# Kernel optimization log

Hardware: AMD Instinct MI355X
Metric: run time of the kernel (lower is better)

The kernel has to match this reference:

```python
import jax, jax.numpy as jnp
import numpy as np

EMBED_DIM = 1024
NUM_HEADS = 16
HEAD_DIM = EMBED_DIM // NUM_HEADS


def setup_inputs() -> dict:
    key = jax.random.key(0)
    ks = jax.random.split(key, 9)
    s = 1.0 / np.sqrt(EMBED_DIM)
    x = jax.random.normal(ks[0], (2, 2048, EMBED_DIM), dtype=jnp.float32)
    Wq = jax.random.uniform(ks[1], (EMBED_DIM, EMBED_DIM), jnp.float32, -s, s)
    bq = jax.random.uniform(ks[2], (EMBED_DIM,), jnp.float32, -s, s)
    Wk = jax.random.uniform(ks[3], (EMBED_DIM, EMBED_DIM), jnp.float32, -s, s)
    bk = jax.random.uniform(ks[4], (EMBED_DIM,), jnp.float32, -s, s)
    Wv = jax.random.uniform(ks[5], (EMBED_DIM, EMBED_DIM), jnp.float32, -s, s)
    bv = jax.random.uniform(ks[6], (EMBED_DIM,), jnp.float32, -s, s)
    Wo = jax.random.uniform(ks[7], (EMBED_DIM, EMBED_DIM), jnp.float32, -s, s)
    bo = jax.random.uniform(ks[8], (EMBED_DIM,), jnp.float32, -s, s)
    return {"x": x, "Wq": Wq, "bq": bq, "Wk": Wk, "bk": bk,
            "Wv": Wv, "bv": bv, "Wo": Wo, "bo": bo}


def reference(x, Wq, bq, Wk, bk, Wv, bv, Wo, bo):
    B, S, E = x.shape
    H, D = NUM_HEADS, HEAD_DIM
    # Linear projections (torch Linear: y = x @ W.T + b; here W stored as [in,out])
    Q = (x @ Wq + bq).reshape(B, S, H, D).transpose(0, 2, 1, 3)  # [B,H,S,D]
    K = (x @ Wk + bk).reshape(B, S, H, D).transpose(0, 2, 1, 3)
    V = (x @ Wv + bv).reshape(B, S, H, D).transpose(0, 2, 1, 3)
    scale = jnp.sqrt(jnp.asarray(D, dtype=jnp.float32))
    energy = jnp.einsum("bhqd,bhkd->bhqk", Q, K) / scale  # [B,H,S,S]
    attn = jax.nn.softmax(energy, axis=-1)
    out = jnp.einsum("bhqk,bhkd->bhqd", attn, V)  # [B,H,S,D]
    out = out.transpose(0, 2, 1, 3).reshape(B, S, E)
    return out @ Wo + bo
```

## Files before the change

### kernel.cpp

```cpp
#include <hip/hip_runtime.h>
#include <cstdint>
#include <cstddef>

#define S_LEN 2048
#define NHEAD 16
#define HDIM  64
#define EMB   1024
#define MROWS 4096
#define KDIM  1024

typedef __bf16 bf16;
typedef unsigned int u32;
typedef __attribute__((ext_vector_type(8)))  __bf16 bf16x8;
typedef __attribute__((ext_vector_type(4)))  __bf16 bf16x4;
typedef __attribute__((ext_vector_type(4)))  float  f32x4;
typedef __attribute__((ext_vector_type(16))) float  f32x16;
typedef __attribute__((ext_vector_type(4)))  u32    u32x4;

__device__ __forceinline__ f32x4 mfma_16x16x32(bf16x8 a, bf16x8 b, f32x4 c) {
  return __builtin_amdgcn_mfma_f32_16x16x32_bf16(a, b, c, 0, 0, 0);
}
__device__ __forceinline__ f32x16 mfma32(bf16x8 a, bf16x8 b, f32x16 c) {
  return __builtin_amdgcn_mfma_f32_32x32x16_bf16(a, b, c, 0, 0, 0);
}
__device__ __forceinline__ u32 cvt_pk_bf16(float lo, float hi) {
  u32 r;
  asm("v_cvt_pk_bf16_f32 %0, %1, %2" : "=v"(r) : "v"(lo), "v"(hi));
  return r;
}
__device__ __forceinline__ f32x16 fz16() {
  f32x16 z;
#pragma unroll
  for (int i = 0; i < 16; i++) z[i] = 0.f;
  return z;
}

__device__ __forceinline__ void gload16(const bf16* g, void* lds_uniform) {
  __builtin_amdgcn_global_load_lds(
      (const __attribute__((address_space(1))) void*)g,
      (__attribute__((address_space(3))) void*)lds_uniform, 16, 0, 0);
}

__global__ void prep_x_kernel(const float* __restrict__ x, bf16* __restrict__ xb) {
  int idx = blockIdx.x * blockDim.x + threadIdx.x;
  const float4* x4 = (const float4*)x;
  float4 a = x4[idx * 2 + 0];
  float4 b = x4[idx * 2 + 1];
  bf16x8 v;
  v[0] = (bf16)a.x; v[1] = (bf16)a.y; v[2] = (bf16)a.z; v[3] = (bf16)a.w;
  v[4] = (bf16)b.x; v[5] = (bf16)b.y; v[6] = (bf16)b.z; v[7] = (bf16)b.w;
  *(bf16x8*)(xb + (size_t)idx * 8) = v;
}

__global__ void prep_w_kernel(const float* __restrict__ Wq, const float* __restrict__ Wk,
                              const float* __restrict__ Wv, const float* __restrict__ Wo,
                              bf16* __restrict__ wqkvt, bf16* __restrict__ wot) {
  __shared__ float tile[64][65];
  int mat = blockIdx.z;
  const float* W = (mat == 0) ? Wq : (mat == 1) ? Wk : (mat == 2) ? Wv : Wo;
  bf16* dst = (mat < 3) ? (wqkvt + (size_t)mat * 1024 * 1024) : wot;
  int k0 = blockIdx.x * 64, r0 = blockIdx.y * 64;
  int tid = threadIdx.x;
#pragma unroll
  for (int i = 0; i < 16; i++) {
    int idx = i * 256 + tid;
    int kk = idx >> 6, rr = idx & 63;
    tile[kk][rr] = W[(size_t)(k0 + kk) * 1024 + r0 + rr];
  }
  __syncthreads();
#pragma unroll
  for (int i = 0; i < 16; i++) {
    int idx = i * 256 + tid;
    int rr = idx >> 6, kk = idx & 63;
    dst[(size_t)(r0 + rr) * 1024 + k0 + kk] = (bf16)tile[kk][rr];
  }
}

template <int MODE>
__global__ __launch_bounds__(256, 2) void gemm_bt(
    const bf16* __restrict__ A, const bf16* __restrict__ Bt,
    const float* __restrict__ b0, const float* __restrict__ b1, const float* __restrict__ b2,
    float* __restrict__ outf,
    bf16* __restrict__ qo, bf16* __restrict__ ko, bf16* __restrict__ vto) {
  __shared__ bf16 lA[128 * 64];
  __shared__ bf16 lB[128 * 64];
  const int bm = blockIdx.x, bn = blockIdx.y;
  const int tid = threadIdx.x;
  const int w = tid >> 6, l = tid & 63;
  const int wm = w >> 1, wn = w & 1;
  const int lr = l & 15, lg = l >> 4;

  f32x4 zero = {0.f, 0.f, 0.f, 0.f};
  f32x4 acc[4][4];
#pragma unroll
  for (int i = 0; i < 4; i++)
#pragma unroll
    for (int j = 0; j < 4; j++) acc[i][j] = zero;

  char* lAb = (char*)lA;
  char* lBb = (char*)lB;
  const size_t a_row0 = (size_t)bm * 128;
  const size_t b_row0 = (size_t)bn * 128;

  for (int kt = 0; kt < KDIM; kt += 64) {
    __syncthreads();
#pragma unroll
    for (int i = 0; i < 4; i++) {
      int cq = i * 256 + tid;
      int row = cq >> 3;
      int c8 = (cq & 7) ^ (row & 7);
      gload16(A + (a_row0 + row) * KDIM + kt + c8 * 8, lAb + (i * 256 + w * 64) * 16);
    }
#pragma unroll
    for (int i = 0; i < 4; i++) {
      int cq = i * 256 + tid;
      int row = cq >> 3;
      int c8 = (cq & 7) ^ (row & 7);
      gload16(Bt + (b_row0 + row) * KDIM + kt + c8 * 8, lBb + (i * 256 + w * 64) * 16);
    }
    asm volatile("s_waitcnt vmcnt(0)" ::: "memory");
    __syncthreads();

#pragma unroll
    for (int kk = 0; kk < 2; kk++) {
      bf16x8 af[4], bfv[4];
#pragma unroll
      for (int i = 0; i < 4; i++) {
        int row = wm * 64 + i * 16 + lr;
        af[i] = *(const bf16x8*)(lAb + row * 128 + ((((kk << 2) + lg) ^ (row & 7)) << 4));
      }
#pragma unroll
      for (int j = 0; j < 4; j++) {
        int row = wn * 64 + j * 16 + lr;
        bfv[j] = *(const bf16x8*)(lBb + row * 128 + ((((kk << 2) + lg) ^ (row & 7)) << 4));
      }
#pragma unroll
      for (int i = 0; i < 4; i++)
#pragma unroll
        for (int j = 0; j < 4; j++) acc[i][j] = mfma_16x16x32(af[i], bfv[j], acc[i][j]);
    }
  }

#pragma unroll
  for (int i = 0; i < 4; i++) {
#pragma unroll
    for (int j = 0; j < 4; j++) {
      int n = bn * 128 + wn * 64 + j * 16 + lr;
      int mbase = bm * 128 + wm * 64 + i * 16 + lg * 4;
      if (MODE == 1) {
#pragma unroll
        for (int jj = 0; jj < 4; jj++)
          outf[(size_t)(mbase + jj) * 1024 + n] = acc[i][j][jj] + b0[n];
      } else {
        int p = n >> 10, nn = n & 1023;
        int h = nn >> 6, d = nn & 63;
        int b = mbase >> 11, s = mbase & 2047;
        const float* bp = (p == 0) ? b0 : (p == 1) ? b1 : b2;
        float bias = bp[nn];
        if (p == 2) {
          bf16x4 pk;
#pragma unroll
          for (int jj = 0; jj < 4; jj++) pk[jj] = (bf16)(acc[i][j][jj] + bias);
          *(bf16x4*)(vto + (((size_t)(b * 16 + h)) * 64 + d) * 2048 + s) = pk;
        } else {
          float qsc = (p == 0) ? 0.18033688011112042f : 1.0f;
          bf16* o = (p == 0) ? qo : ko;
#pragma unroll
          for (int jj = 0; jj < 4; jj++)
            o[(((size_t)(b * 16 + h)) * 2048 + s + jj) * 64 + d] =
                (bf16)((acc[i][j][jj] + bias) * qsc);
        }
      }
    }
  }
}

__global__ __launch_bounds__(256, 2) void attn_kernel(
    const bf16* __restrict__ qb, const bf16* __restrict__ kb,
    const bf16* __restrict__ vtb, bf16* __restrict__ ob) {
  __shared__ bf16 lKV[4 * 8192];
  const int bid = blockIdx.x;
  const int work = ((bid & 7) << 6) | (bid >> 3);
  const int qt = work & 15;
  const int bh = work >> 4;
  const int tid = threadIdx.x;
  const int w = tid >> 6, l = tid & 63;
  const int l5 = l >> 5, l31 = l & 31;

  const bf16* Qh = qb + (size_t)bh * S_LEN * HDIM;
  const bf16* Kh = kb + (size_t)bh * S_LEN * HDIM;
  const bf16* Vh = vtb + (size_t)bh * HDIM * S_LEN;

  const int qrow = qt * 128 + w * 32 + l31;
  const bf16* qp = Qh + (size_t)qrow * 64 + l5 * 8;
  bf16x8 qf0 = *(const bf16x8*)(qp);
  bf16x8 qf1 = *(const bf16x8*)(qp + 16);
  bf16x8 qf2 = *(const bf16x8*)(qp + 32);
  bf16x8 qf3 = *(const bf16x8*)(qp + 48);

  bf16x8 ones;
#pragma unroll
  for (int i = 0; i < 8; i++) ones[i] = (bf16)1.0f;

  f32x16 o0 = fz16(), o1 = fz16(), lsum = fz16();

  char* lb = (char*)lKV;

  const int rb = l31 * 128;
  const int xb_ = 4 * ((l31 >> 3) & 1);
  const int cso0 = (((0 + l5) ^ (l & 7) ^ xb_) << 4);
  const int cso1 = (((2 + l5) ^ (l & 7) ^ xb_) << 4);
  const int cso2 = (((4 + l5) ^ (l & 7) ^ xb_) << 4);
  const int cso3 = (((6 + l5) ^ (l & 7) ^ xb_) << 4);

  const int row0 = tid >> 3;
  const int c8e = (((tid & 7) ^ (row0 & 7) ^ (4 * ((row0 >> 3) & 1))) << 3);
  int koff = row0 * HDIM + c8e;
  int voff = row0 * S_LEN + c8e;
  char* lkd = lb + w * 1024;
  char* lvd = lb + 8192 + w * 1024;

#define STAGE(B)                                                              \
  {                                                                           \
    gload16(Kh + koff,         lkd + (B));                                    \
    gload16(Kh + koff + 2048,  lkd + (B) + 4096);                             \
    gload16(Vh + voff,         lvd + (B));                                    \
    gload16(Vh + voff + 65536, lvd + (B) + 4096);                             \
    koff += 4096;                                                             \
    voff += 64;                                                               \
  }

#define QKHALF(B, H, paA, paB)                                                \
  {                                                                           \
    const char* kB_ = lb + (B) + (H) * 4096;                                  \
    f32x16 s = fz16();                                                        \
    __builtin_amdgcn_s_setprio(1);                                            \
    bf16x8 kf0 = *(const bf16x8*)(kB_ + rb + cso0);                           \
    bf16x8 kf1 = *(const bf16x8*)(kB_ + rb + cso1);                           \
    bf16x8 kf2 = *(const bf16x8*)(kB_ + rb + cso2);                           \
    bf16x8 kf3 = *(const bf16x8*)(kB_ + rb + cso3);                           \
    s = mfma32(kf0, qf0, s);                                                  \
    s = mfma32(kf1, qf1, s);                                                  \
    s = mfma32(kf2, qf2, s);                                                  \
    s = mfma32(kf3, qf3, s);                                                  \
    __builtin_amdgcn_s_setprio(0);                                            \
    _Pragma("unroll") for (int r = 0; r < 16; r++)                            \
      s[r] = __builtin_amdgcn_exp2f(s[r]);                                    \
    {                                                                         \
      u32 a_ = cvt_pk_bf16(s[0], s[1]);                                       \
      u32 b_ = cvt_pk_bf16(s[2], s[3]);                                       \
      u32 c_ = cvt_pk_bf16(s[4], s[5]);                                       \
      u32 d_ = cvt_pk_bf16(s[6], s[7]);                                       \
      asm("v_permlane32_swap_b32 %0, %1" : "+v"(a_), "+v"(c_));               \
      asm("v_permlane32_swap_b32 %0, %1" : "+v"(b_), "+v"(d_));               \
      u32x4 t_ = {a_, b_, c_, d_};                                            \
      paA = __builtin_bit_cast(bf16x8, t_);                                   \
    }                                                                         \
    {                                                                         \
      u32 a_ = cvt_pk_bf16(s[8], s[9]);                                       \
      u32 b_ = cvt_pk_bf16(s[10], s[11]);                                     \
      u32 c_ = cvt_pk_bf16(s[12], s[13]);                                     \
      u32 d_ = cvt_pk_bf16(s[14], s[15]);                                     \
      asm("v_permlane32_swap_b32 %0, %1" : "+v"(a_), "+v"(c_));               \
      asm("v_permlane32_swap_b32 %0, %1" : "+v"(b_), "+v"(d_));               \
      u32x4 t_ = {a_, b_, c_, d_};                                            \
      paB = __builtin_bit_cast(bf16x8, t_);                                   \
    }                                                                         \
  }

#define COMPUTE(B)                                                            \
  {                                                                           \
    bf16x8 pa0, pa1, pa2, pa3;                                                \
    QKHALF(B, 0, pa0, pa1);                                                   \
    QKHALF(B, 1, pa2, pa3);                                                   \
    const char* vB_ = lb + (B) + 8192;                                        \
    __builtin_amdgcn_s_setprio(1);                                            \
    lsum = mfma32(pa0, ones, lsum);                                           \
    lsum = mfma32(pa1, ones, lsum);                                           \
    lsum = mfma32(pa2, ones, lsum);                                           \
    lsum = mfma32(pa3, ones, lsum);                                           \
    {                                                                         \
      bf16x8 vf0 = *(const bf16x8*)(vB_ + rb + cso0);                         \
      bf16x8 vf1 = *(const bf16x8*)(vB_ + rb + cso1);                         \
      bf16x8 vf2 = *(const bf16x8*)(vB_ + rb + cso2);                         \
      bf16x8 vf3 = *(const bf16x8*)(vB_ + rb + cso3);                         \
      o0 = mfma32(pa0, vf0, o0);                                              \
      o0 = mfma32(pa1, vf1, o0);                                              \
      o0 = mfma32(pa2, vf2, o0);                                              \
      o0 = mfma32(pa3, vf3, o0);                                              \
    }                                                                         \
    {                                                                         \
      bf16x8 vf0 = *(const bf16x8*)(vB_ + 4096 + rb + cso0);                  \
      bf16x8 vf1 = *(const bf16x8*)(vB_ + 4096 + rb + cso1);                  \
      bf16x8 vf2 = *(const bf16x8*)(vB_ + 4096 + rb + cso2);                  \
      bf16x8 vf3 = *(const bf16x8*)(vB_ + 4096 + rb + cso3);                  \
      o1 = mfma32(pa0, vf0, o1);                                              \
      o1 = mfma32(pa1, vf1, o1);                                              \
      o1 = mfma32(pa2, vf2, o1);                                              \
      o1 = mfma32(pa3, vf3, o1);                                              \
    }                                                                         \
    __builtin_amdgcn_s_setprio(0);                                            \
  }

  STAGE(0 << 14);
  STAGE(1 << 14);
  STAGE(2 << 14);

  for (int t = 0; t < 30; ++t) {
    asm volatile("s_waitcnt vmcnt(8)" ::: "memory");
    __builtin_amdgcn_s_barrier();
    __builtin_amdgcn_sched_barrier(0);
    if (t < 29) STAGE(((t + 3) & 3) << 14);
    COMPUTE((t & 3) << 14);
  }
  asm volatile("s_waitcnt vmcnt(4)" ::: "memory");
  __builtin_amdgcn_s_barrier();
  __builtin_amdgcn_sched_barrier(0);
  COMPUTE(2 << 14);
  asm volatile("s_waitcnt vmcnt(0)" ::: "memory");
  __builtin_amdgcn_s_barrier();
  __builtin_amdgcn_sched_barrier(0);
  COMPUTE(3 << 14);

#undef STAGE
#undef QKHALF
#undef COMPUTE

  const int b = bh >> 4, h = bh & 15;
#pragma unroll
  for (int r = 0; r < 16; r++) {
    int q = (r & 3) + 8 * (r >> 2) + 4 * l5;
    int s = qt * 128 + w * 32 + q;
    float inv = 1.0f / lsum[r];
    size_t base = ((size_t)(b * 2048 + s)) * 1024 + h * 64 + l31;
    ob[base]      = (bf16)(o0[r] * inv);
    ob[base + 32] = (bf16)(o1[r] * inv);
  }
}

extern "C" void kernel_launch(void* const* d_in, const int* in_sizes, int n_in,
                              void* d_out, int out_size, void* d_ws, size_t ws_size,
                              hipStream_t stream) {
  const float* x  = (const float*)d_in[0];
  const float* Wq = (const float*)d_in[1];
  const float* bq = (const float*)d_in[2];
  const float* Wk = (const float*)d_in[3];
  const float* bk = (const float*)d_in[4];
  const float* Wv = (const float*)d_in[5];
  const float* bv = (const float*)d_in[6];
  const float* Wo = (const float*)d_in[7];
  const float* bo = (const float*)d_in[8];
  float* out = (float*)d_out;

  char* ws = (char*)d_ws;
  bf16* xb    = (bf16*)(ws + (size_t)(0)  * (1 << 20));
  bf16* wqkvt = (bf16*)(ws + (size_t)(8)  * (1 << 20));
  bf16* wot   = (bf16*)(ws + (size_t)(14) * (1 << 20));
  bf16* qbuf  = (bf16*)(ws + (size_t)(16) * (1 << 20));
  bf16* kbuf  = (bf16*)(ws + (size_t)(24) * (1 << 20));
  bf16* vtbuf = (bf16*)(ws + (size_t)(32) * (1 << 20));
  bf16* obuf  = (bf16*)(ws + (size_t)(40) * (1 << 20));

  prep_x_kernel<<<dim3(2048), dim3(256), 0, stream>>>(x, xb);
  prep_w_kernel<<<dim3(16, 16, 4), dim3(256), 0, stream>>>(Wq, Wk, Wv, Wo, wqkvt, wot);
  gemm_bt<0><<<dim3(32, 24), dim3(256), 0, stream>>>(xb, wqkvt, bq, bk, bv,
                                                     nullptr, qbuf, kbuf, vtbuf);
  attn_kernel<<<dim3(512), dim3(256), 0, stream>>>(qbuf, kbuf, vtbuf, obuf);
  gemm_bt<1><<<dim3(32, 8), dim3(256), 0, stream>>>(obuf, wot, bo, nullptr, nullptr,
                                                    out, nullptr, nullptr, nullptr);
}
```

Measured before the change: 102.3 us.

## Split attention KV range across two blocks and combine partial outputs

Each (batch, head, query-tile) is now processed by two blocks, each covering half of the key/value sequence, which doubles the grid to 1024 blocks. The LDS ring buffer shrinks from four stages to two so that four blocks can be resident per CU. Unnormalized partial outputs and row sums go to workspace, and a new combine kernel adds the two halves and normalizes them. The aim is better occupancy and CU utilization. The cost is a shallower load pipeline that waits on vmcnt(0) every step, extra global traffic for the partials, and one more kernel launch.

```diff
diff --git a/kernel.cpp b/kernel.cpp
--- a/kernel.cpp
+++ b/kernel.cpp
@@ -175,14 +175,16 @@
   }
 }
 
-__global__ __launch_bounds__(256, 2) void attn_kernel(
+__global__ __launch_bounds__(256, 4) void attn_kernel(
     const bf16* __restrict__ qb, const bf16* __restrict__ kb,
-    const bf16* __restrict__ vtb, bf16* __restrict__ ob) {
-  __shared__ bf16 lKV[4 * 8192];
+    const bf16* __restrict__ vtb, bf16* __restrict__ po0, bf16* __restrict__ po1,
+    float* __restrict__ plb) {
+  __shared__ bf16 lKV[2 * 8192];
   const int bid = blockIdx.x;
-  const int work = ((bid & 7) << 6) | (bid >> 3);
+  const int work = ((bid & 7) << 7) | (bid >> 3);
   const int qt = work & 15;
-  const int bh = work >> 4;
+  const int bh = (work >> 4) & 31;
+  const int sp = work >> 9;
   const int tid = threadIdx.x;
   const int w = tid >> 6, l = tid & 63;
   const int l5 = l >> 5, l31 = l & 31;
@@ -215,8 +217,8 @@
 
   const int row0 = tid >> 3;
   const int c8e = (((tid & 7) ^ (row0 & 7) ^ (4 * ((row0 >> 3) & 1))) << 3);
-  int koff = row0 * HDIM + c8e;
-  int voff = row0 * S_LEN + c8e;
+  int koff = row0 * HDIM + c8e + sp * 65536;
+  int voff = row0 * S_LEN + c8e + sp * 1024;
   char* lkd = lb + w * 1024;
   char* lvd = lb + 8192 + w * 1024;
 
@@ -302,40 +304,51 @@
     __builtin_amdgcn_s_setprio(0);                                            \
   }
 
-  STAGE(0 << 14);
-  STAGE(1 << 14);
-  STAGE(2 << 14);
-
-  for (int t = 0; t < 30; ++t) {
-    asm volatile("s_waitcnt vmcnt(8)" ::: "memory");
+  STAGE(0);
+
+  for (int t = 0; t < 16; ++t) {
+    asm volatile("s_waitcnt vmcnt(0)" ::: "memory");
     __builtin_amdgcn_s_barrier();
     __builtin_amdgcn_sched_barrier(0);
-    if (t < 29) STAGE(((t + 3) & 3) << 14);
-    COMPUTE((t & 3) << 14);
-  }
-  asm volatile("s_waitcnt vmcnt(4)" ::: "memory");
-  __builtin_amdgcn_s_barrier();
-  __builtin_amdgcn_sched_barrier(0);
-  COMPUTE(2 << 14);
-  asm volatile("s_waitcnt vmcnt(0)" ::: "memory");
-  __builtin_amdgcn_s_barrier();
-  __builtin_amdgcn_sched_barrier(0);
-  COMPUTE(3 << 14);
+    if (t < 15) STAGE(((t + 1) & 1) << 14);
+    COMPUTE((t & 1) << 14);
+  }
 
 #undef STAGE
 #undef QKHALF
 #undef COMPUTE
 
-  const int b = bh >> 4, h = bh & 15;
+  bf16* po = (sp == 0) ? po0 : po1;
+  float* pl = plb + sp * 65536;
+  const int bb = bh >> 4, h = bh & 15;
+  const int srow0 = qt * 128 + w * 32;
 #pragma unroll
   for (int r = 0; r < 16; r++) {
     int q = (r & 3) + 8 * (r >> 2) + 4 * l5;
-    int s = qt * 128 + w * 32 + q;
-    float inv = 1.0f / lsum[r];
-    size_t base = ((size_t)(b * 2048 + s)) * 1024 + h * 64 + l31;
-    ob[base]      = (bf16)(o0[r] * inv);
-    ob[base + 32] = (bf16)(o1[r] * inv);
-  }
+    int s = srow0 + q;
+    size_t base = ((size_t)(bb * 2048 + s)) * 1024 + h * 64 + l31;
+    po[base]      = (bf16)o0[r];
+    po[base + 32] = (bf16)o1[r];
+    if (l31 == 0) pl[(bh << 11) + s] = lsum[r];
+  }
+}
+
+__global__ void combine_kernel(const bf16* __restrict__ po0, const float* __restrict__ plb,
+                               bf16* __restrict__ ob) {
+  int idx = blockIdx.x * blockDim.x + threadIdx.x;
+  size_t e = (size_t)idx * 8;
+  int m = idx >> 7;
+  int h = (idx & 127) >> 3;
+  int b = m >> 11, s = m & 2047;
+  int lrow = ((b * 16 + h) << 11) + s;
+  float inv = 1.0f / (plb[lrow] + plb[lrow + 65536]);
+  bf16x8 a = *(const bf16x8*)(po0 + e);
+  bf16x8 c = *(const bf16x8*)(ob + e);
+  bf16x8 v;
+#pragma unroll
+  for (int i = 0; i < 8; i++)
+    v[i] = (bf16)(((float)a[i] + (float)c[i]) * inv);
+  *(bf16x8*)(ob + e) = v;
 }
 
 extern "C" void kernel_launch(void* const* d_in, const int* in_sizes, int n_in,
@@ -360,12 +373,15 @@
   bf16* kbuf  = (bf16*)(ws + (size_t)(24) * (1 << 20));
   bf16* vtbuf = (bf16*)(ws + (size_t)(32) * (1 << 20));
   bf16* obuf  = (bf16*)(ws + (size_t)(40) * (1 << 20));
+  bf16* po0   = (bf16*)(ws + (size_t)(0)  * (1 << 20));
+  float* plb  = (float*)(ws + (size_t)(8) * (1 << 20));
 
   prep_x_kernel<<<dim3(2048), dim3(256), 0, stream>>>(x, xb);
   prep_w_kernel<<<dim3(16, 16, 4), dim3(256), 0, stream>>>(Wq, Wk, Wv, Wo, wqkvt, wot);
   gemm_bt<0><<<dim3(32, 24), dim3(256), 0, stream>>>(xb, wqkvt, bq, bk, bv,
                                                      nullptr, qbuf, kbuf, vtbuf);
-  attn_kernel<<<dim3(512), dim3(256), 0, stream>>>(qbuf, kbuf, vtbuf, obuf);
+  attn_kernel<<<dim3(1024), dim3(256), 0, stream>>>(qbuf, kbuf, vtbuf, po0, obuf, plb);
+  combine_kernel<<<dim3(2048), dim3(256), 0, stream>>>(po0, plb, obuf);
   gemm_bt<1><<<dim3(32, 8), dim3(256), 0, stream>>>(obuf, wot, bo, nullptr, nullptr,
                                                     out, nullptr, nullptr, nullptr);
 }
```

Result: slower. 106.6 us (+4.2%).
